# Optimization experiments

Hardware: AMD Instinct MI355X
Metric: run time of the kernel (lower is better)

Reference implementation:

```python
import jax, jax.numpy as jnp
import numpy as np

HIST_LEN = 100  # STDP history cap in the original module


def setup_inputs() -> dict:
    key = jax.random.key(0)
    ks = jax.random.split(key, 5)
    H, B = 1024, 16384
    return {
        "x": jax.random.normal(ks[0], (B, H), dtype=jnp.float32),
        "weights": jax.random.normal(ks[1], (H, H), dtype=jnp.float32) * 0.1,
        "meta_plasticity": jnp.ones((H,), dtype=jnp.float32),
        "pre_hist": jax.random.normal(ks[2], (HIST_LEN, H), dtype=jnp.float32) * 0.1,
        "post_hist": jax.random.normal(ks[3], (HIST_LEN, H), dtype=jnp.float32) * 0.1,
        "activity_history": jnp.zeros((1000,), dtype=jnp.float32),
        "history_pointer": 5,
        "stdp_window": jnp.float32(20.0),
        "stdp_decay": jnp.float32(0.1),
        "target_activity": jnp.float32(0.1),
        "homeostatic_rate": jnp.float32(0.01),
        "meta_learning_rate": jnp.float32(0.001),
    }


def reference(x, weights, meta_plasticity, pre_hist, post_hist,
              activity_history, history_pointer, stdp_window, stdp_decay,
              target_activity, homeostatic_rate, meta_learning_rate):
    # --- forward matmul: weights * meta_plasticity scales columns (broadcast over rows)
    output = x @ (weights * meta_plasticity)  # [B, H]

    # --- STDP update (vectorized form of the python loop over the history) ---
    # append current mean activities, pop oldest (steady-state length == HIST_LEN)
    pre = jnp.concatenate([pre_hist[1:], x.mean(axis=0)[None]], axis=0)       # [L, H]
    post = jnp.concatenate([post_hist[1:], output.mean(axis=0)[None]], axis=0)
    L = HIST_LEN
    i = jnp.arange(L, dtype=jnp.float32)
    dt = (L - i) * stdp_window
    w = 0.01 * jnp.exp(-dt * stdp_decay)                                      # [L]
    pos_w = jnp.where(i < L - 1, w, 0.0)   # i < len-1 branch
    neg_w = jnp.where(i > 0, w, 0.0)       # i > 0 branch
    # sum_i pos_w[i] * outer(post[-1], pre[i]) = outer(post[-1], pos_w @ pre)
    dW = jnp.outer(post[-1], pos_w @ pre) - jnp.outer(neg_w @ post, pre[-1])
    new_w = jnp.clip(weights + dW, -1.0, 1.0)

    # --- homeostatic plasticity ---
    hist = activity_history.at[history_pointer].set(output.mean())
    activity_diff = target_activity - hist.mean()
    new_w = jnp.clip(new_w * (1.0 + homeostatic_rate * activity_diff), -1.0, 1.0)

    # --- meta plasticity ---
    new_meta = jnp.clip(
        meta_plasticity + meta_learning_rate * (output.mean(axis=0) - meta_plasticity),
        0.0, 2.0)

    return output, new_w, new_meta, hist
```

## Files before the change

kernel.cpp:

```cpp
#include <hip/hip_runtime.h>
#include <hip/hip_bf16.h>

#define H 1024
#define BATCH 16384

typedef unsigned short u16;
typedef u16 u16x8 __attribute__((ext_vector_type(8)));
typedef __bf16 bf16x8 __attribute__((ext_vector_type(8)));
typedef float f32x4 __attribute__((ext_vector_type(4)));

typedef __attribute__((address_space(3))) unsigned int lds_uint;
typedef __attribute__((address_space(1))) const unsigned int glob_uint;

__device__ __forceinline__ u16 f2bf(float f) {
  unsigned int u = __float_as_uint(f);
  u += 0x7fffu + ((u >> 16) & 1u);
  return (u16)(u >> 16);
}

#define WS_XSUMP   0
#define WS_XSUM    (WS_XSUMP + 256 * H)
#define WS_ORAWP   (WS_XSUM + H)
#define WS_POSVP   (WS_ORAWP + 16 * H)
#define WS_NEGHP   (WS_POSVP + 5 * H)
#define WS_OUTMEAN (WS_NEGHP + 5 * H)
#define WS_POSV    (WS_OUTMEAN + H)
#define WS_NEGH    (WS_POSV + H)
#define WS_SCALEP  (WS_NEGH + H)
#define WS_BF16    (WS_SCALEP + 16)

__global__ __launch_bounds__(256) void prep_kernel(const float* __restrict__ X,
                                                   const float* __restrict__ W,
                                                   u16* __restrict__ Xb,
                                                   u16* __restrict__ Wbt,
                                                   float* __restrict__ ws,
                                                   const float* __restrict__ pre,
                                                   const float* __restrict__ post,
                                                   const float* __restrict__ win,
                                                   const float* __restrict__ dec) {
  __shared__ __align__(16) u16 t[64][72];
  const int b = blockIdx.x, tid = threadIdx.x;
  if (b < 256) {
    size_t r0 = (size_t)b * 64;
    float s0 = 0.f, s1 = 0.f, s2 = 0.f, s3 = 0.f;
#pragma unroll 4
    for (int r = 0; r < 64; ++r) {
      size_t off = (r0 + r) * H + tid * 4;
      const float4 v = *(const float4*)&X[off];
      ushort4 h;
      h.x = f2bf(v.x); h.y = f2bf(v.y); h.z = f2bf(v.z); h.w = f2bf(v.w);
      *(ushort4*)&Xb[off] = h;
      s0 += v.x; s1 += v.y; s2 += v.z; s3 += v.w;
    }
    float* row = &ws[WS_XSUMP + b * H];
    row[tid * 4 + 0] = s0; row[tid * 4 + 1] = s1;
    row[tid * 4 + 2] = s2; row[tid * 4 + 3] = s3;
  } else if (b < 512) {
    const int b2 = b - 256;
    const int n0 = (b2 & 15) * 64, k0 = (b2 >> 4) * 64;
    const int rb = tid >> 4, c4 = tid & 15;
#pragma unroll
    for (int i = 0; i < 4; ++i) {
      int r = rb + i * 16;
      const float4 v = *(const float4*)&W[(size_t)(k0 + r) * H + n0 + c4 * 4];
      t[c4 * 4 + 0][r] = f2bf(v.x);
      t[c4 * 4 + 1][r] = f2bf(v.y);
      t[c4 * 4 + 2][r] = f2bf(v.z);
      t[c4 * 4 + 3][r] = f2bf(v.w);
    }
    __syncthreads();
    const int seg = tid & 7;
#pragma unroll
    for (int p = 0; p < 2; ++p) {
      int wr = p * 32 + (tid >> 3);
      *(u16x8*)&Wbt[(size_t)(n0 + wr) * H + k0 + seg * 8] = *(const u16x8*)&t[wr][seg * 8];
    }
  } else {
    const int b2 = b - 512;
    const int col = (b2 & 3) * 256 + tid;
    const int seg = b2 >> 2;
    const int t0 = 1 + seg * 20;
    int tend = t0 + 20; if (tend > 100) tend = 100;
    float wd = win[0] * dec[0];
    float ps = 0.f, ns = 0.f;
    for (int tt = t0; tt < tend; ++tt) {
      float w = 0.01f * expf(-(float)(101 - tt) * wd);
      ps += w * pre[tt * H + col];
      if (tt >= 2) ns += w * post[tt * H + col];
    }
    ws[WS_POSVP + seg * H + col] = ps;
    ws[WS_NEGHP + seg * H + col] = ns;
  }
}

__global__ __launch_bounds__(256) void gemm_vm_kernel(const u16* __restrict__ Xb,
                                                      const u16* __restrict__ Wbt,
                                                      const float* __restrict__ meta,
                                                      const float* __restrict__ W,
                                                      float* __restrict__ ws,
                                                      float* __restrict__ out) {
  __shared__ __align__(16) u16 lA[8192];
  __shared__ __align__(16) u16 lB[8192];
  __shared__ float xs[64];

  const int b = blockIdx.x, tid = threadIdx.x;

  if (b < 64) {
    const int jx = b & 3, ky = b >> 2;
    if (tid < 64) {
      float s = 0.f;
      const float* p = &ws[WS_XSUMP + ky * 64 + tid];
#pragma unroll 8
      for (int q = 0; q < 256; ++q) s += p[q * H];
      xs[tid] = s;
      if (jx == 0) ws[WS_XSUM + ky * 64 + tid] = s;
    }
    __syncthreads();
    const int j = jx * 256 + tid;
    float s = 0.f;
#pragma unroll 8
    for (int k = 0; k < 64; ++k) s += xs[k] * W[(size_t)(ky * 64 + k) * H + j];
    ws[WS_ORAWP + ky * H + j] = s * (1.0f / (float)BATCH);
    return;
  }

  const int bg = b - 64;
  const int mt = bg & 127, nt = bg >> 7;
  const size_t row0 = (size_t)mt * 128;
  const int col0 = nt * 128;
  const int wave = tid >> 6;
  const int lane = tid & 63;
  const int quad = lane >> 4;
  const int l16 = lane & 15;
  const int wm = wave >> 1, wn = wave & 1;

  f32x4 acc[4][4];
#pragma unroll
  for (int i = 0; i < 4; ++i)
#pragma unroll
    for (int j = 0; j < 4; ++j) acc[i][j] = (f32x4){0.f, 0.f, 0.f, 0.f};

  for (int k0 = 0; k0 < H; k0 += 64) {
#pragma unroll
    for (int i = 0; i < 4; ++i) {
      const int c = wave * 4 + i;
      const int half = c >> 3;
      const int rr = (c & 7) * 16 + (lane >> 2);
      const int kk = half * 32 + (lane & 3) * 8;
      const u16* ga = &Xb[(row0 + rr) * H + k0 + kk];
      const u16* gb = &Wbt[(size_t)(col0 + rr) * H + k0 + kk];
      u16* la = &lA[half * 4096 + (c & 7) * 512];
      u16* lb = &lB[half * 4096 + (c & 7) * 512];
      __builtin_amdgcn_global_load_lds((glob_uint*)ga, (lds_uint*)la, 16, 0, 0);
      __builtin_amdgcn_global_load_lds((glob_uint*)gb, (lds_uint*)lb, 16, 0, 0);
    }
    __syncthreads();
#pragma unroll
    for (int ks = 0; ks < 2; ++ks) {
      bf16x8 av[4], bv[4];
#pragma unroll
      for (int f = 0; f < 4; ++f) {
        av[f] = __builtin_bit_cast(bf16x8,
            *(const u16x8*)&lA[ks * 4096 + (wm * 64 + f * 16 + l16) * 32 + quad * 8]);
        bv[f] = __builtin_bit_cast(bf16x8,
            *(const u16x8*)&lB[ks * 4096 + (wn * 64 + f * 16 + l16) * 32 + quad * 8]);
      }
#pragma unroll
      for (int fm = 0; fm < 4; ++fm)
#pragma unroll
        for (int fn = 0; fn < 4; ++fn)
          acc[fm][fn] = __builtin_amdgcn_mfma_f32_16x16x32_bf16(av[fm], bv[fn], acc[fm][fn], 0, 0, 0);
    }
    __syncthreads();
  }

  float mcol[4];
#pragma unroll
  for (int fn = 0; fn < 4; ++fn) mcol[fn] = meta[col0 + wn * 64 + fn * 16 + l16];
#pragma unroll
  for (int fm = 0; fm < 4; ++fm) {
#pragma unroll
    for (int fn = 0; fn < 4; ++fn) {
      int col = col0 + wn * 64 + fn * 16 + l16;
#pragma unroll
      for (int r = 0; r < 4; ++r) {
        size_t row = row0 + wm * 64 + fm * 16 + quad * 4 + r;
        out[row * H + col] = acc[fm][fn][r] * mcol[fn];
      }
    }
  }
}

__global__ __launch_bounds__(1024) void finalize2_kernel(const float* __restrict__ meta,
                                                         const float* __restrict__ act,
                                                         const int* __restrict__ ptr,
                                                         const float* __restrict__ targ,
                                                         const float* __restrict__ homeo,
                                                         const float* __restrict__ mlr,
                                                         float* __restrict__ ws,
                                                         float* __restrict__ meta_out,
                                                         float* __restrict__ hist_out) {
  __shared__ float r1[16], r2[16];
  __shared__ float sc[2];
  int t = threadIdx.x;
  float oraw = 0.f;
#pragma unroll
  for (int i = 0; i < 16; ++i) oraw += ws[WS_ORAWP + i * H + t];
  float om = meta[t] * oraw;
  ws[WS_OUTMEAN + t] = om;
  float pv = 0.f, nv = 0.f;
#pragma unroll
  for (int i = 0; i < 5; ++i) { pv += ws[WS_POSVP + i * H + t]; nv += ws[WS_NEGHP + i * H + t]; }
  ws[WS_POSV + t] = pv;
  ws[WS_NEGH + t] = nv;

  float a = (t < 1000) ? act[t] : 0.f;
  float s1 = om, s2 = a;
#pragma unroll
  for (int o = 32; o > 0; o >>= 1) {
    s1 += __shfl_down(s1, o, 64);
    s2 += __shfl_down(s2, o, 64);
  }
  if ((t & 63) == 0) { r1[t >> 6] = s1; r2[t >> 6] = s2; }
  __syncthreads();
  if (t == 0) {
    float ts1 = 0.f, ts2 = 0.f;
#pragma unroll
    for (int i = 0; i < 16; ++i) { ts1 += r1[i]; ts2 += r2[i]; }
    float total_mean = ts1 / (float)H;
    int p = ptr[0];
    float hist_mean = (ts2 - act[p] + total_mean) / 1000.f;
    float diff = targ[0] - hist_mean;
    sc[0] = 1.f + homeo[0] * diff;
    sc[1] = total_mean;
    ws[WS_SCALEP] = sc[0];
  }
  __syncthreads();
  float nm = meta[t] + mlr[0] * (om - meta[t]);
  nm = fminf(fmaxf(nm, 0.f), 2.f);
  meta_out[t] = nm;
  if (t < 1000) hist_out[t] = (t == ptr[0]) ? sc[1] : act[t];
}

__global__ __launch_bounds__(256) void neww_kernel(const float* __restrict__ W,
                                                   const float* __restrict__ outmean,
                                                   const float* __restrict__ posv,
                                                   const float* __restrict__ negh,
                                                   const float* __restrict__ xsum,
                                                   const float* __restrict__ scalep,
                                                   const float* __restrict__ win,
                                                   const float* __restrict__ dec,
                                                   float* __restrict__ out) {
  int idx4 = blockIdx.x * 256 + threadIdx.x;
  int rr = idx4 >> 8;
  int c4 = (idx4 & 255) * 4;
  float w99 = 0.01f * expf(-win[0] * dec[0]);
  float scale = scalep[0];
  float om_r = outmean[rr];
  float neg_r = negh[rr] + w99 * om_r;
  const float4 wv = *(const float4*)&W[(size_t)rr * H + c4];
  const float4 pv = *(const float4*)&posv[c4];
  const float4 xv = *(const float4*)&xsum[c4];
  float4 o;
  float vx[4] = {wv.x, wv.y, wv.z, wv.w};
  float px[4] = {pv.x, pv.y, pv.z, pv.w};
  float xx[4] = {xv.x, xv.y, xv.z, xv.w};
  float ox[4];
#pragma unroll
  for (int i = 0; i < 4; ++i) {
    float v = vx[i] + om_r * px[i] - neg_r * (xx[i] * (1.0f / (float)BATCH));
    v = fminf(fmaxf(v, -1.f), 1.f);
    v = v * scale;
    ox[i] = fminf(fmaxf(v, -1.f), 1.f);
  }
  o.x = ox[0]; o.y = ox[1]; o.z = ox[2]; o.w = ox[3];
  *(float4*)&out[(size_t)rr * H + c4] = o;
}

__global__ __launch_bounds__(256) void colsum_kernel(const float* __restrict__ x,
                                                     float* __restrict__ xsum) {
  int col = blockIdx.x * 256 + threadIdx.x;
  size_t r0 = (size_t)blockIdx.y * 256;
  float s = 0.f;
#pragma unroll 8
  for (int r = 0; r < 256; ++r) s += x[(r0 + r) * H + col];
  atomicAdd(&xsum[col], s);
}

__global__ __launch_bounds__(256) void gemm_fallback_kernel(const float* __restrict__ X,
                                                            const float* __restrict__ W,
                                                            const float* __restrict__ meta,
                                                            float* __restrict__ out) {
  __shared__ __align__(16) u16 lA[128][40];
  __shared__ __align__(16) u16 lB[128][40];
  const int tid = threadIdx.x;
  const int wave = tid >> 6;
  const int lane = tid & 63;
  const int quad = lane >> 4;
  const int l16 = lane & 15;
  const int wm = wave >> 1, wn = wave & 1;
  const size_t row0 = (size_t)blockIdx.x * 128;
  const int col0 = blockIdx.y * 128;
  f32x4 acc[4][4];
#pragma unroll
  for (int i = 0; i < 4; ++i)
#pragma unroll
    for (int j = 0; j < 4; ++j) acc[i][j] = (f32x4){0.f, 0.f, 0.f, 0.f};
  for (int k0 = 0; k0 < H; k0 += 32) {
#pragma unroll
    for (int i = 0; i < 4; ++i) {
      int idx = i * 256 + tid;
      int r = idx >> 3, c4 = idx & 7;
      const float4 v = *(const float4*)&X[(row0 + r) * H + k0 + c4 * 4];
      ushort4 h;
      h.x = f2bf(v.x); h.y = f2bf(v.y); h.z = f2bf(v.z); h.w = f2bf(v.w);
      *(ushort4*)&lA[r][c4 * 4] = h;
    }
#pragma unroll
    for (int i = 0; i < 4; ++i) {
      int idx = i * 256 + tid;
      int kk = idx >> 5, c4 = idx & 31;
      const float4 v = *(const float4*)&W[(size_t)(k0 + kk) * H + col0 + c4 * 4];
      lB[c4 * 4 + 0][kk] = f2bf(v.x);
      lB[c4 * 4 + 1][kk] = f2bf(v.y);
      lB[c4 * 4 + 2][kk] = f2bf(v.z);
      lB[c4 * 4 + 3][kk] = f2bf(v.w);
    }
    __syncthreads();
    bf16x8 av[4], bv[4];
#pragma unroll
    for (int f = 0; f < 4; ++f) {
      av[f] = __builtin_bit_cast(bf16x8, *(const u16x8*)&lA[wm * 64 + f * 16 + l16][quad * 8]);
      bv[f] = __builtin_bit_cast(bf16x8, *(const u16x8*)&lB[wn * 64 + f * 16 + l16][quad * 8]);
    }
#pragma unroll
    for (int fm = 0; fm < 4; ++fm)
#pragma unroll
      for (int fn = 0; fn < 4; ++fn)
        acc[fm][fn] = __builtin_amdgcn_mfma_f32_16x16x32_bf16(av[fm], bv[fn], acc[fm][fn], 0, 0, 0);
    __syncthreads();
  }
  float mcol[4];
#pragma unroll
  for (int fn = 0; fn < 4; ++fn) mcol[fn] = meta[col0 + wn * 64 + fn * 16 + l16];
#pragma unroll
  for (int fm = 0; fm < 4; ++fm) {
#pragma unroll
    for (int fn = 0; fn < 4; ++fn) {
      int col = col0 + wn * 64 + fn * 16 + l16;
#pragma unroll
      for (int r = 0; r < 4; ++r) {
        size_t row = row0 + wm * 64 + fm * 16 + quad * 4 + r;
        out[row * H + col] = acc[fm][fn][r] * mcol[fn];
      }
    }
  }
}

__global__ __launch_bounds__(256) void vecmat_kernel(const float* __restrict__ W,
                                                     const float* __restrict__ xsum,
                                                     float* __restrict__ outraw) {
  int j = blockIdx.x * 256 + threadIdx.x;
  int k0 = blockIdx.y * 64;
  float s = 0.f;
#pragma unroll 8
  for (int k = 0; k < 64; ++k) s += xsum[k0 + k] * W[(size_t)(k0 + k) * H + j];
  atomicAdd(&outraw[j], s * (1.0f / (float)BATCH));
}

__global__ __launch_bounds__(256) void stdpvec_kernel(const float* __restrict__ pre,
                                                      const float* __restrict__ post,
                                                      const float* __restrict__ win,
                                                      const float* __restrict__ dec,
                                                      float* __restrict__ posv,
                                                      float* __restrict__ negh) {
  int col = blockIdx.x * 256 + threadIdx.x;
  int t0 = 1 + blockIdx.y * 20;
  float wd = win[0] * dec[0];
  float ps = 0.f, ns = 0.f;
  int tend = t0 + 20;
  if (tend > 100) tend = 100;
  for (int t = t0; t < tend; ++t) {
    float w = 0.01f * expf(-(float)(101 - t) * wd);
    ps += w * pre[t * H + col];
    if (t >= 2) ns += w * post[t * H + col];
  }
  atomicAdd(&posv[col], ps);
  atomicAdd(&negh[col], ns);
}

__global__ __launch_bounds__(1024) void finalize_kernel(const float* __restrict__ meta,
                                                        const float* __restrict__ act,
                                                        const int* __restrict__ ptr,
                                                        const float* __restrict__ targ,
                                                        const float* __restrict__ homeo,
                                                        const float* __restrict__ mlr,
                                                        const float* __restrict__ outraw,
                                                        float* __restrict__ outmean,
                                                        float* __restrict__ scalep,
                                                        float* __restrict__ meta_out,
                                                        float* __restrict__ hist_out) {
  __shared__ float r1[16], r2[16];
  __shared__ float sc[2];
  int t = threadIdx.x;
  float om = meta[t] * outraw[t];
  outmean[t] = om;
  float a = (t < 1000) ? act[t] : 0.f;
  float s1 = om, s2 = a;
#pragma unroll
  for (int o = 32; o > 0; o >>= 1) {
    s1 += __shfl_down(s1, o, 64);
    s2 += __shfl_down(s2, o, 64);
  }
  if ((t & 63) == 0) { r1[t >> 6] = s1; r2[t >> 6] = s2; }
  __syncthreads();
  if (t == 0) {
    float ts1 = 0.f, ts2 = 0.f;
#pragma unroll
    for (int i = 0; i < 16; ++i) { ts1 += r1[i]; ts2 += r2[i]; }
    float total_mean = ts1 / (float)H;
    int p = ptr[0];
    float hist_mean = (ts2 - act[p] + total_mean) / 1000.f;
    float diff = targ[0] - hist_mean;
    sc[0] = 1.f + homeo[0] * diff;
    sc[1] = total_mean;
    scalep[0] = sc[0];
  }
  __syncthreads();
  float nm = meta[t] + mlr[0] * (om - meta[t]);
  nm = fminf(fmaxf(nm, 0.f), 2.f);
  meta_out[t] = nm;
  if (t < 1000) hist_out[t] = (t == ptr[0]) ? sc[1] : act[t];
}

extern "C" void kernel_launch(void* const* d_in, const int* in_sizes, int n_in,
                              void* d_out, int out_size, void* d_ws, size_t ws_size,
                              hipStream_t stream) {
  const float* x     = (const float*)d_in[0];
  const float* W     = (const float*)d_in[1];
  const float* meta  = (const float*)d_in[2];
  const float* pre   = (const float*)d_in[3];
  const float* post  = (const float*)d_in[4];
  const float* act   = (const float*)d_in[5];
  const int*   ptr   = (const int*)d_in[6];
  const float* win   = (const float*)d_in[7];
  const float* dec   = (const float*)d_in[8];
  const float* targ  = (const float*)d_in[9];
  const float* homeo = (const float*)d_in[10];
  const float* mlr   = (const float*)d_in[11];

  float* out_y    = (float*)d_out;
  float* out_w    = out_y + (size_t)BATCH * H;
  float* out_meta = out_w + (size_t)H * H;
  float* out_hist = out_meta + H;

  float* ws = (float*)d_ws;
  u16* Xb  = (u16*)(ws + WS_BF16);
  u16* Wbt = Xb + (size_t)BATCH * H;

  const size_t ws_need = (size_t)WS_BF16 * sizeof(float) +
                         ((size_t)BATCH * H + (size_t)H * H) * sizeof(u16);

  if (ws_size >= ws_need) {
    prep_kernel<<<532, 256, 0, stream>>>(x, W, Xb, Wbt, ws, pre, post, win, dec);
    gemm_vm_kernel<<<1088, 256, 0, stream>>>(Xb, Wbt, meta, W, ws, out_y);
    finalize2_kernel<<<1, 1024, 0, stream>>>(meta, act, ptr, targ, homeo, mlr,
                                             ws, out_meta, out_hist);
    neww_kernel<<<1024, 256, 0, stream>>>(W, ws + WS_OUTMEAN, ws + WS_POSV, ws + WS_NEGH,
                                          ws + WS_XSUM, ws + WS_SCALEP, win, dec, out_w);
  } else {
    float* xsum    = ws;
    float* outraw  = ws + 1024;
    float* outmean = ws + 2048;
    float* posv    = ws + 3072;
    float* negh    = ws + 4096;
    float* scalep  = ws + 5120;
    hipMemsetAsync(d_ws, 0, 6144 * sizeof(float), stream);
    colsum_kernel<<<dim3(4, 64), 256, 0, stream>>>(x, xsum);
    gemm_fallback_kernel<<<dim3(128, 8), 256, 0, stream>>>(x, W, meta, out_y);
    vecmat_kernel<<<dim3(4, 16), 256, 0, stream>>>(W, xsum, outraw);
    stdpvec_kernel<<<dim3(4, 5), 256, 0, stream>>>(pre, post, win, dec, posv, negh);
    finalize_kernel<<<1, 1024, 0, stream>>>(meta, act, ptr, targ, homeo, mlr,
                                            outraw, outmean, scalep, out_meta, out_hist);
    neww_kernel<<<1024, 256, 0, stream>>>(W, outmean, posv, negh, xsum, scalep, win, dec, out_w);
  }
}
```

Baseline: 224.7 us.

## Fuse finalize and weight-update into one tail kernel; shrink GEMM K-tile to 32

Merges the single-block finalize kernel and the new-weight kernel into one 1024-block tail kernel. Each block redundantly recomputes the global output mean, homeostatic scale and per-row STDP terms from the partial sums, which removes one launch and one serialized single-block step. The GEMM main loop also moves from 64-wide to 32-wide K tiles, halving LDS use but doubling barrier count per tile. The fallback kernels are only moved, not changed.

```diff
diff --git a/kernel.cpp b/kernel.cpp
--- a/kernel.cpp
+++ b/kernel.cpp
@@ -23,11 +23,8 @@
 #define WS_ORAWP   (WS_XSUM + H)
 #define WS_POSVP   (WS_ORAWP + 16 * H)
 #define WS_NEGHP   (WS_POSVP + 5 * H)
-#define WS_OUTMEAN (WS_NEGHP + 5 * H)
-#define WS_POSV    (WS_OUTMEAN + H)
-#define WS_NEGH    (WS_POSV + H)
-#define WS_SCALEP  (WS_NEGH + H)
-#define WS_BF16    (WS_SCALEP + 16)
+#define WS_SCRATCH (WS_NEGHP + 5 * H)
+#define WS_BF16    (WS_SCRATCH + 16)
 
 __global__ __launch_bounds__(256) void prep_kernel(const float* __restrict__ X,
                                                    const float* __restrict__ W,
@@ -99,8 +96,8 @@
                                                       const float* __restrict__ W,
                                                       float* __restrict__ ws,
                                                       float* __restrict__ out) {
-  __shared__ __align__(16) u16 lA[8192];
-  __shared__ __align__(16) u16 lB[8192];
+  __shared__ __align__(16) u16 lA[128 * 32];
+  __shared__ __align__(16) u16 lB[128 * 32];
   __shared__ float xs[64];
 
   const int b = blockIdx.x, tid = threadIdx.x;
@@ -134,43 +131,37 @@
   const int l16 = lane & 15;
   const int wm = wave >> 1, wn = wave & 1;
 
+  const int sr = lane >> 2;
+  const int sk = (lane & 3) * 8;
+
   f32x4 acc[4][4];
 #pragma unroll
   for (int i = 0; i < 4; ++i)
 #pragma unroll
     for (int j = 0; j < 4; ++j) acc[i][j] = (f32x4){0.f, 0.f, 0.f, 0.f};
 
-  for (int k0 = 0; k0 < H; k0 += 64) {
-#pragma unroll
-    for (int i = 0; i < 4; ++i) {
-      const int c = wave * 4 + i;
-      const int half = c >> 3;
-      const int rr = (c & 7) * 16 + (lane >> 2);
-      const int kk = half * 32 + (lane & 3) * 8;
-      const u16* ga = &Xb[(row0 + rr) * H + k0 + kk];
-      const u16* gb = &Wbt[(size_t)(col0 + rr) * H + k0 + kk];
-      u16* la = &lA[half * 4096 + (c & 7) * 512];
-      u16* lb = &lB[half * 4096 + (c & 7) * 512];
-      __builtin_amdgcn_global_load_lds((glob_uint*)ga, (lds_uint*)la, 16, 0, 0);
-      __builtin_amdgcn_global_load_lds((glob_uint*)gb, (lds_uint*)lb, 16, 0, 0);
+  for (int k0 = 0; k0 < H; k0 += 32) {
+#pragma unroll
+    for (int i = 0; i < 2; ++i) {
+      const int rg = i * 64 + wave * 16;
+      const u16* ga = &Xb[(row0 + rg + sr) * H + k0 + sk];
+      const u16* gb = &Wbt[(size_t)(col0 + rg + sr) * H + k0 + sk];
+      __builtin_amdgcn_global_load_lds((glob_uint*)ga, (lds_uint*)&lA[rg * 32], 16, 0, 0);
+      __builtin_amdgcn_global_load_lds((glob_uint*)gb, (lds_uint*)&lB[rg * 32], 16, 0, 0);
     }
     __syncthreads();
-#pragma unroll
-    for (int ks = 0; ks < 2; ++ks) {
-      bf16x8 av[4], bv[4];
-#pragma unroll
-      for (int f = 0; f < 4; ++f) {
-        av[f] = __builtin_bit_cast(bf16x8,
-            *(const u16x8*)&lA[ks * 4096 + (wm * 64 + f * 16 + l16) * 32 + quad * 8]);
-        bv[f] = __builtin_bit_cast(bf16x8,
-            *(const u16x8*)&lB[ks * 4096 + (wn * 64 + f * 16 + l16) * 32 + quad * 8]);
-      }
-#pragma unroll
-      for (int fm = 0; fm < 4; ++fm)
-#pragma unroll
-        for (int fn = 0; fn < 4; ++fn)
-          acc[fm][fn] = __builtin_amdgcn_mfma_f32_16x16x32_bf16(av[fm], bv[fn], acc[fm][fn], 0, 0, 0);
-    }
+
+    bf16x8 av[4], bv[4];
+#pragma unroll
+    for (int f = 0; f < 4; ++f) {
+      av[f] = __builtin_bit_cast(bf16x8, *(const u16x8*)&lA[(wm * 64 + f * 16 + l16) * 32 + quad * 8]);
+      bv[f] = __builtin_bit_cast(bf16x8, *(const u16x8*)&lB[(wn * 64 + f * 16 + l16) * 32 + quad * 8]);
+    }
+#pragma unroll
+    for (int fm = 0; fm < 4; ++fm)
+#pragma unroll
+      for (int fn = 0; fn < 4; ++fn)
+        acc[fm][fn] = __builtin_amdgcn_mfma_f32_16x16x32_bf16(av[fm], bv[fn], acc[fm][fn], 0, 0, 0);
     __syncthreads();
   }
 
@@ -191,29 +182,235 @@
   }
 }
 
-__global__ __launch_bounds__(1024) void finalize2_kernel(const float* __restrict__ meta,
-                                                         const float* __restrict__ act,
-                                                         const int* __restrict__ ptr,
-                                                         const float* __restrict__ targ,
-                                                         const float* __restrict__ homeo,
-                                                         const float* __restrict__ mlr,
-                                                         float* __restrict__ ws,
-                                                         float* __restrict__ meta_out,
-                                                         float* __restrict__ hist_out) {
+__global__ __launch_bounds__(256) void tail_kernel(const float* __restrict__ W,
+                                                   const float* __restrict__ meta,
+                                                   const float* __restrict__ act,
+                                                   const int* __restrict__ ptr,
+                                                   const float* __restrict__ targ,
+                                                   const float* __restrict__ homeo,
+                                                   const float* __restrict__ mlr,
+                                                   const float* __restrict__ win,
+                                                   const float* __restrict__ dec,
+                                                   const float* __restrict__ ws,
+                                                   float* __restrict__ out_w,
+                                                   float* __restrict__ meta_out,
+                                                   float* __restrict__ hist_out) {
+  __shared__ float r1[4], r2[4];
+  const int r = blockIdx.x;
+  const int t = threadIdx.x;
+  const int c4 = t * 4;
+
+  f32x4 oraw = (f32x4){0.f, 0.f, 0.f, 0.f};
+#pragma unroll
+  for (int i = 0; i < 16; ++i) {
+    const float4 v = *(const float4*)&ws[WS_ORAWP + i * H + c4];
+    oraw[0] += v.x; oraw[1] += v.y; oraw[2] += v.z; oraw[3] += v.w;
+  }
+  const float4 mv = *(const float4*)&meta[c4];
+  f32x4 om;
+  om[0] = mv.x * oraw[0]; om[1] = mv.y * oraw[1];
+  om[2] = mv.z * oraw[2]; om[3] = mv.w * oraw[3];
+
+  float s1 = om[0] + om[1] + om[2] + om[3];
+  float s2 = 0.f;
+#pragma unroll
+  for (int j = 0; j < 4; ++j) {
+    int idx = t + j * 256;
+    if (idx < 1000) s2 += act[idx];
+  }
+#pragma unroll
+  for (int o = 32; o > 0; o >>= 1) {
+    s1 += __shfl_down(s1, o, 64);
+    s2 += __shfl_down(s2, o, 64);
+  }
+  if ((t & 63) == 0) { r1[t >> 6] = s1; r2[t >> 6] = s2; }
+  __syncthreads();
+  const float ts1 = r1[0] + r1[1] + r1[2] + r1[3];
+  const float ts2 = r2[0] + r2[1] + r2[2] + r2[3];
+  const float total_mean = ts1 / (float)H;
+  const int p = ptr[0];
+  const float hist_mean = (ts2 - act[p] + total_mean) / 1000.f;
+  const float scale = 1.f + homeo[0] * (targ[0] - hist_mean);
+  const float w99 = 0.01f * expf(-win[0] * dec[0]);
+
+  float oraw_r = 0.f;
+#pragma unroll
+  for (int i = 0; i < 16; ++i) oraw_r += ws[WS_ORAWP + i * H + r];
+  const float om_r = meta[r] * oraw_r;
+  float negh_r = 0.f;
+#pragma unroll
+  for (int i = 0; i < 5; ++i) negh_r += ws[WS_NEGHP + i * H + r];
+  const float neg_r = negh_r + w99 * om_r;
+
+  f32x4 pv = (f32x4){0.f, 0.f, 0.f, 0.f};
+#pragma unroll
+  for (int i = 0; i < 5; ++i) {
+    const float4 v = *(const float4*)&ws[WS_POSVP + i * H + c4];
+    pv[0] += v.x; pv[1] += v.y; pv[2] += v.z; pv[3] += v.w;
+  }
+  const float4 xv = *(const float4*)&ws[WS_XSUM + c4];
+  float xx[4] = {xv.x, xv.y, xv.z, xv.w};
+  const float4 wv = *(const float4*)&W[(size_t)r * H + c4];
+  float wx[4] = {wv.x, wv.y, wv.z, wv.w};
+  float4 o;
+  float ox[4];
+#pragma unroll
+  for (int i = 0; i < 4; ++i) {
+    float v = wx[i] + om_r * pv[i] - neg_r * (xx[i] * (1.0f / (float)BATCH));
+    v = fminf(fmaxf(v, -1.f), 1.f);
+    v = v * scale;
+    ox[i] = fminf(fmaxf(v, -1.f), 1.f);
+  }
+  o.x = ox[0]; o.y = ox[1]; o.z = ox[2]; o.w = ox[3];
+  *(float4*)&out_w[(size_t)r * H + c4] = o;
+
+  if (r == 0) {
+    float4 nm;
+    float nx[4] = {mv.x, mv.y, mv.z, mv.w};
+    float nr[4];
+#pragma unroll
+    for (int i = 0; i < 4; ++i) {
+      float v = nx[i] + mlr[0] * (om[i] - nx[i]);
+      nr[i] = fminf(fmaxf(v, 0.f), 2.f);
+    }
+    nm.x = nr[0]; nm.y = nr[1]; nm.z = nr[2]; nm.w = nr[3];
+    *(float4*)&meta_out[c4] = nm;
+#pragma unroll
+    for (int j = 0; j < 4; ++j) {
+      int idx = t + j * 256;
+      if (idx < 1000) hist_out[idx] = (idx == p) ? total_mean : act[idx];
+    }
+  }
+}
+
+__global__ __launch_bounds__(256) void colsum_kernel(const float* __restrict__ x,
+                                                     float* __restrict__ xsum) {
+  int col = blockIdx.x * 256 + threadIdx.x;
+  size_t r0 = (size_t)blockIdx.y * 256;
+  float s = 0.f;
+#pragma unroll 8
+  for (int r = 0; r < 256; ++r) s += x[(r0 + r) * H + col];
+  atomicAdd(&xsum[col], s);
+}
+
+__global__ __launch_bounds__(256) void gemm_fallback_kernel(const float* __restrict__ X,
+                                                            const float* __restrict__ W,
+                                                            const float* __restrict__ meta,
+                                                            float* __restrict__ out) {
+  __shared__ __align__(16) u16 lA[128][40];
+  __shared__ __align__(16) u16 lB[128][40];
+  const int tid = threadIdx.x;
+  const int wave = tid >> 6;
+  const int lane = tid & 63;
+  const int quad = lane >> 4;
+  const int l16 = lane & 15;
+  const int wm = wave >> 1, wn = wave & 1;
+  const size_t row0 = (size_t)blockIdx.x * 128;
+  const int col0 = blockIdx.y * 128;
+  f32x4 acc[4][4];
+#pragma unroll
+  for (int i = 0; i < 4; ++i)
+#pragma unroll
+    for (int j = 0; j < 4; ++j) acc[i][j] = (f32x4){0.f, 0.f, 0.f, 0.f};
+  for (int k0 = 0; k0 < H; k0 += 32) {
+#pragma unroll
+    for (int i = 0; i < 4; ++i) {
+      int idx = i * 256 + tid;
+      int r = idx >> 3, c4 = idx & 7;
+      const float4 v = *(const float4*)&X[(row0 + r) * H + k0 + c4 * 4];
+      ushort4 h;
+      h.x = f2bf(v.x); h.y = f2bf(v.y); h.z = f2bf(v.z); h.w = f2bf(v.w);
+      *(ushort4*)&lA[r][c4 * 4] = h;
+    }
+#pragma unroll
+    for (int i = 0; i < 4; ++i) {
+      int idx = i * 256 + tid;
+      int kk = idx >> 5, c4 = idx & 31;
+      const float4 v = *(const float4*)&W[(size_t)(k0 + kk) * H + col0 + c4 * 4];
+      lB[c4 * 4 + 0][kk] = f2bf(v.x);
+      lB[c4 * 4 + 1][kk] = f2bf(v.y);
+      lB[c4 * 4 + 2][kk] = f2bf(v.z);
+      lB[c4 * 4 + 3][kk] = f2bf(v.w);
+    }
+    __syncthreads();
+    bf16x8 av[4], bv[4];
+#pragma unroll
+    for (int f = 0; f < 4; ++f) {
+      av[f] = __builtin_bit_cast(bf16x8, *(const u16x8*)&lA[wm * 64 + f * 16 + l16][quad * 8]);
+      bv[f] = __builtin_bit_cast(bf16x8, *(const u16x8*)&lB[wn * 64 + f * 16 + l16][quad * 8]);
+    }
+#pragma unroll
+    for (int fm = 0; fm < 4; ++fm)
+#pragma unroll
+      for (int fn = 0; fn < 4; ++fn)
+        acc[fm][fn] = __builtin_amdgcn_mfma_f32_16x16x32_bf16(av[fm], bv[fn], acc[fm][fn], 0, 0, 0);
+    __syncthreads();
+  }
+  float mcol[4];
+#pragma unroll
+  for (int fn = 0; fn < 4; ++fn) mcol[fn] = meta[col0 + wn * 64 + fn * 16 + l16];
+#pragma unroll
+  for (int fm = 0; fm < 4; ++fm) {
+#pragma unroll
+    for (int fn = 0; fn < 4; ++fn) {
+      int col = col0 + wn * 64 + fn * 16 + l16;
+#pragma unroll
+      for (int r = 0; r < 4; ++r) {
+        size_t row = row0 + wm * 64 + fm * 16 + quad * 4 + r;
+        out[row * H + col] = acc[fm][fn][r] * mcol[fn];
+      }
+    }
+  }
+}
+
+__global__ __launch_bounds__(256) void vecmat_kernel(const float* __restrict__ W,
+                                                     const float* __restrict__ xsum,
+                                                     float* __restrict__ outraw) {
+  int j = blockIdx.x * 256 + threadIdx.x;
+  int k0 = blockIdx.y * 64;
+  float s = 0.f;
+#pragma unroll 8
+  for (int k = 0; k < 64; ++k) s += xsum[k0 + k] * W[(size_t)(k0 + k) * H + j];
+  atomicAdd(&outraw[j], s * (1.0f / (float)BATCH));
+}
+
+__global__ __launch_bounds__(256) void stdpvec_kernel(const float* __restrict__ pre,
+                                                      const float* __restrict__ post,
+                                                      const float* __restrict__ win,
+                                                      const float* __restrict__ dec,
+                                                      float* __restrict__ posv,
+                                                      float* __restrict__ negh) {
+  int col = blockIdx.x * 256 + threadIdx.x;
+  int t0 = 1 + blockIdx.y * 20;
+  float wd = win[0] * dec[0];
+  float ps = 0.f, ns = 0.f;
+  int tend = t0 + 20;
+  if (tend > 100) tend = 100;
+  for (int t = t0; t < tend; ++t) {
+    float w = 0.01f * expf(-(float)(101 - t) * wd);
+    ps += w * pre[t * H + col];
+    if (t >= 2) ns += w * post[t * H + col];
+  }
+  atomicAdd(&posv[col], ps);
+  atomicAdd(&negh[col], ns);
+}
+
+__global__ __launch_bounds__(1024) void finalize_kernel(const float* __restrict__ meta,
+                                                        const float* __restrict__ act,
+                                                        const int* __restrict__ ptr,
+                                                        const float* __restrict__ targ,
+                                                        const float* __restrict__ homeo,
+                                                        const float* __restrict__ mlr,
+                                                        const float* __restrict__ outraw,
+                                                        float* __restrict__ outmean,
+                                                        float* __restrict__ scalep,
+                                                        float* __restrict__ meta_out,
+                                                        float* __restrict__ hist_out) {
   __shared__ float r1[16], r2[16];
   __shared__ float sc[2];
   int t = threadIdx.x;
-  float oraw = 0.f;
-#pragma unroll
-  for (int i = 0; i < 16; ++i) oraw += ws[WS_ORAWP + i * H + t];
-  float om = meta[t] * oraw;
-  ws[WS_OUTMEAN + t] = om;
-  float pv = 0.f, nv = 0.f;
-#pragma unroll
-  for (int i = 0; i < 5; ++i) { pv += ws[WS_POSVP + i * H + t]; nv += ws[WS_NEGHP + i * H + t]; }
-  ws[WS_POSV + t] = pv;
-  ws[WS_NEGH + t] = nv;
-
+  float om = meta[t] * outraw[t];
+  outmean[t] = om;
   float a = (t < 1000) ? act[t] : 0.f;
   float s1 = om, s2 = a;
 #pragma unroll
@@ -233,7 +430,7 @@
     float diff = targ[0] - hist_mean;
     sc[0] = 1.f + homeo[0] * diff;
     sc[1] = total_mean;
-    ws[WS_SCALEP] = sc[0];
+    scalep[0] = sc[0];
   }
   __syncthreads();
   float nm = meta[t] + mlr[0] * (om - meta[t]);
@@ -277,162 +474,6 @@
   *(float4*)&out[(size_t)rr * H + c4] = o;
 }
 
-__global__ __launch_bounds__(256) void colsum_kernel(const float* __restrict__ x,
-                                                     float* __restrict__ xsum) {
-  int col = blockIdx.x * 256 + threadIdx.x;
-  size_t r0 = (size_t)blockIdx.y * 256;
-  float s = 0.f;
-#pragma unroll 8
-  for (int r = 0; r < 256; ++r) s += x[(r0 + r) * H + col];
-  atomicAdd(&xsum[col], s);
-}
-
-__global__ __launch_bounds__(256) void gemm_fallback_kernel(const float* __restrict__ X,
-                                                            const float* __restrict__ W,
-                                                            const float* __restrict__ meta,
-                                                            float* __restrict__ out) {
-  __shared__ __align__(16) u16 lA[128][40];
-  __shared__ __align__(16) u16 lB[128][40];
-  const int tid = threadIdx.x;
-  const int wave = tid >> 6;
-  const int lane = tid & 63;
-  const int quad = lane >> 4;
-  const int l16 = lane & 15;
-  const int wm = wave >> 1, wn = wave & 1;
-  const size_t row0 = (size_t)blockIdx.x * 128;
-  const int col0 = blockIdx.y * 128;
-  f32x4 acc[4][4];
-#pragma unroll
-  for (int i = 0; i < 4; ++i)
-#pragma unroll
-    for (int j = 0; j < 4; ++j) acc[i][j] = (f32x4){0.f, 0.f, 0.f, 0.f};
-  for (int k0 = 0; k0 < H; k0 += 32) {
-#pragma unroll
-    for (int i = 0; i < 4; ++i) {
-      int idx = i * 256 + tid;
-      int r = idx >> 3, c4 = idx & 7;
-      const float4 v = *(const float4*)&X[(row0 + r) * H + k0 + c4 * 4];
-      ushort4 h;
-      h.x = f2bf(v.x); h.y = f2bf(v.y); h.z = f2bf(v.z); h.w = f2bf(v.w);
-      *(ushort4*)&lA[r][c4 * 4] = h;
-    }
-#pragma unroll
-    for (int i = 0; i < 4; ++i) {
-      int idx = i * 256 + tid;
-      int kk = idx >> 5, c4 = idx & 31;
-      const float4 v = *(const float4*)&W[(size_t)(k0 + kk) * H + col0 + c4 * 4];
-      lB[c4 * 4 + 0][kk] = f2bf(v.x);
-      lB[c4 * 4 + 1][kk] = f2bf(v.y);
-      lB[c4 * 4 + 2][kk] = f2bf(v.z);
-      lB[c4 * 4 + 3][kk] = f2bf(v.w);
-    }
-    __syncthreads();
-    bf16x8 av[4], bv[4];
-#pragma unroll
-    for (int f = 0; f < 4; ++f) {
-      av[f] = __builtin_bit_cast(bf16x8, *(const u16x8*)&lA[wm * 64 + f * 16 + l16][quad * 8]);
-      bv[f] = __builtin_bit_cast(bf16x8, *(const u16x8*)&lB[wn * 64 + f * 16 + l16][quad * 8]);
-    }
-#pragma unroll
-    for (int fm = 0; fm < 4; ++fm)
-#pragma unroll
-      for (int fn = 0; fn < 4; ++fn)
-        acc[fm][fn] = __builtin_amdgcn_mfma_f32_16x16x32_bf16(av[fm], bv[fn], acc[fm][fn], 0, 0, 0);
-    __syncthreads();
-  }
-  float mcol[4];
-#pragma unroll
-  for (int fn = 0; fn < 4; ++fn) mcol[fn] = meta[col0 + wn * 64 + fn * 16 + l16];
-#pragma unroll
-  for (int fm = 0; fm < 4; ++fm) {
-#pragma unroll
-    for (int fn = 0; fn < 4; ++fn) {
-      int col = col0 + wn * 64 + fn * 16 + l16;
-#pragma unroll
-      for (int r = 0; r < 4; ++r) {
-        size_t row = row0 + wm * 64 + fm * 16 + quad * 4 + r;
-        out[row * H + col] = acc[fm][fn][r] * mcol[fn];
-      }
-    }
-  }
-}
-
-__global__ __launch_bounds__(256) void vecmat_kernel(const float* __restrict__ W,
-                                                     const float* __restrict__ xsum,
-                                                     float* __restrict__ outraw) {
-  int j = blockIdx.x * 256 + threadIdx.x;
-  int k0 = blockIdx.y * 64;
-  float s = 0.f;
-#pragma unroll 8
-  for (int k = 0; k < 64; ++k) s += xsum[k0 + k] * W[(size_t)(k0 + k) * H + j];
-  atomicAdd(&outraw[j], s * (1.0f / (float)BATCH));
-}
-
-__global__ __launch_bounds__(256) void stdpvec_kernel(const float* __restrict__ pre,
-                                                      const float* __restrict__ post,
-                                                      const float* __restrict__ win,
-                                                      const float* __restrict__ dec,
-                                                      float* __restrict__ posv,
-                                                      float* __restrict__ negh) {
-  int col = blockIdx.x * 256 + threadIdx.x;
-  int t0 = 1 + blockIdx.y * 20;
-  float wd = win[0] * dec[0];
-  float ps = 0.f, ns = 0.f;
-  int tend = t0 + 20;
-  if (tend > 100) tend = 100;
-  for (int t = t0; t < tend; ++t) {
-    float w = 0.01f * expf(-(float)(101 - t) * wd);
-    ps += w * pre[t * H + col];
-    if (t >= 2) ns += w * post[t * H + col];
-  }
-  atomicAdd(&posv[col], ps);
-  atomicAdd(&negh[col], ns);
-}
-
-__global__ __launch_bounds__(1024) void finalize_kernel(const float* __restrict__ meta,
-                                                        const float* __restrict__ act,
-                                                        const int* __restrict__ ptr,
-                                                        const float* __restrict__ targ,
-                                                        const float* __restrict__ homeo,
-                                                        const float* __restrict__ mlr,
-                                                        const float* __restrict__ outraw,
-                                                        float* __restrict__ outmean,
-                                                        float* __restrict__ scalep,
-                                                        float* __restrict__ meta_out,
-                                                        float* __restrict__ hist_out) {
-  __shared__ float r1[16], r2[16];
-  __shared__ float sc[2];
-  int t = threadIdx.x;
-  float om = meta[t] * outraw[t];
-  outmean[t] = om;
-  float a = (t < 1000) ? act[t] : 0.f;
-  float s1 = om, s2 = a;
-#pragma unroll
-  for (int o = 32; o > 0; o >>= 1) {
-    s1 += __shfl_down(s1, o, 64);
-    s2 += __shfl_down(s2, o, 64);
-  }
-  if ((t & 63) == 0) { r1[t >> 6] = s1; r2[t >> 6] = s2; }
-  __syncthreads();
-  if (t == 0) {
-    float ts1 = 0.f, ts2 = 0.f;
-#pragma unroll
-    for (int i = 0; i < 16; ++i) { ts1 += r1[i]; ts2 += r2[i]; }
-    float total_mean = ts1 / (float)H;
-    int p = ptr[0];
-    float hist_mean = (ts2 - act[p] + total_mean) / 1000.f;
-    float diff = targ[0] - hist_mean;
-    sc[0] = 1.f + homeo[0] * diff;
-    sc[1] = total_mean;
-    scalep[0] = sc[0];
-  }
-  __syncthreads();
-  float nm = meta[t] + mlr[0] * (om - meta[t]);
-  nm = fminf(fmaxf(nm, 0.f), 2.f);
-  meta_out[t] = nm;
-  if (t < 1000) hist_out[t] = (t == ptr[0]) ? sc[1] : act[t];
-}
-
 extern "C" void kernel_launch(void* const* d_in, const int* in_sizes, int n_in,
                               void* d_out, int out_size, void* d_ws, size_t ws_size,
                               hipStream_t stream) {
@@ -464,10 +505,8 @@
   if (ws_size >= ws_need) {
     prep_kernel<<<532, 256, 0, stream>>>(x, W, Xb, Wbt, ws, pre, post, win, dec);
     gemm_vm_kernel<<<1088, 256, 0, stream>>>(Xb, Wbt, meta, W, ws, out_y);
-    finalize2_kernel<<<1, 1024, 0, stream>>>(meta, act, ptr, targ, homeo, mlr,
-                                             ws, out_meta, out_hist);
-    neww_kernel<<<1024, 256, 0, stream>>>(W, ws + WS_OUTMEAN, ws + WS_POSV, ws + WS_NEGH,
-                                          ws + WS_XSUM, ws + WS_SCALEP, win, dec, out_w);
+    tail_kernel<<<1024, 256, 0, stream>>>(W, meta, act, ptr, targ, homeo, mlr,
+                                          win, dec, ws, out_w, out_meta, out_hist);
   } else {
     float* xsum    = ws;
     float* outraw  = ws + 1024;
```

Result: faster. 214.9 us (-4.4%).
